# Kernel tuning notes

Hardware: AMD Instinct MI355X
Metric: run time of the kernel (lower is better)

The kernel has to match this reference:

```python
import jax, jax.numpy as jnp
import numpy as np

N_ROWS = 8192
EMBED = 256


def setup_inputs() -> dict:
    key = jax.random.key(0)
    k1, k2, k3, k4, k5 = jax.random.split(key, 5)
    M = jax.random.normal(k1, (N_ROWS, EMBED), dtype=jnp.float32)
    N = jax.random.normal(k2, (N_ROWS, EMBED), dtype=jnp.float32)
    gate_w_weight = jax.random.normal(k3, (1, EMBED), dtype=jnp.float32) * (1.0 / np.sqrt(EMBED))
    gate_w_bias = jax.random.normal(k4, (1,), dtype=jnp.float32)
    gate_b = jax.random.normal(k5, (1,), dtype=jnp.float32)
    return {"M": M, "N": N, "gate_w_weight": gate_w_weight,
            "gate_w_bias": gate_w_bias, "gate_b": gate_b}


def reference(M, N, gate_w_weight, gate_w_bias, gate_b):
    # scores: [n, n] = N @ M^T
    mt = jnp.matmul(N, M.T)
    # zero the diagonal (mt - diag(diag(mt)))
    n = mt.shape[0]
    idx = jnp.arange(n)
    diag_zeroed = mt.at[idx, idx].set(0.0)
    attn = jax.nn.softmax(diag_zeroed, axis=-1)
    out_attn = jnp.matmul(attn, M)  # [n, d]
    # gate: Linear(d -> 1) + extra scalar bias, then sigmoid
    gate_tmp = jnp.matmul(out_attn, gate_w_weight.T) + gate_w_bias + gate_b  # [n, 1]
    gate = jax.nn.sigmoid(gate_tmp)
    boosted = out_attn * gate + N * (1.0 - gate)
    return boosted[:, None, None, :]  # [n, 1, 1, d]
```

## Files before the change

kernel.cpp:

```cpp
#include <hip/hip_runtime.h>
#include <math.h>

#define NR   8192
#define DIM  256
#define QBLK 32

using f32x4  = __attribute__((ext_vector_type(4))) float;
using s4v    = __attribute__((ext_vector_type(4))) short;
using s8v    = __attribute__((ext_vector_type(8))) short;
using bf16x8 = __attribute__((ext_vector_type(8))) short;
typedef _Float16 f16x8 __attribute__((ext_vector_type(8)));
typedef _Float16 f16x4 __attribute__((ext_vector_type(4)));

__device__ __forceinline__ short f2bf(float x){
  union{float f; unsigned u;} v; v.f = x;
  unsigned r = v.u + 0x7fffu + ((v.u >> 16) & 1u);
  return (short)(r >> 16);
}
__device__ __forceinline__ float bf2f(short s){
  union{unsigned u; float f;} v; v.u = ((unsigned)(unsigned short)s) << 16;
  return v.f;
}
__device__ __forceinline__ short f2h(float x){
  union{_Float16 h; short s;} c; c.h = (_Float16)x; return c.s;
}

#define SS_SHORTS 32768
#define WS_BYTES_NEEDED (128u * 32768u * 2u)

#define LDS6_SHORTS 65536

__device__ __forceinline__ void dma16(const short* g, short* l){
  __builtin_amdgcn_global_load_lds(
      (const __attribute__((address_space(1))) unsigned int*)g,
      (__attribute__((address_space(3))) unsigned int*)l, 16, 0, 0);
}

__launch_bounds__(256)
__global__ void precompute_ws(const float* __restrict__ Mp, short* __restrict__ ws)
{
  const int tid = threadIdx.x;
  const int bx  = blockIdx.x;
  const int ss  = bx >> 4;
  const int sub = bx & 15;
  const int fi  = sub*256 + tid;
  const int plane = fi >> 11;
  const int rest  = fi & 2047;
  const int p   = rest >> 10;
  const int cl  = rest & 1023;
  const int ch  = cl >> 6;
  const int l   = cl & 63;
  const int li  = l & 15, g = l >> 4;

  short v[8];
  if (plane == 0){
    const int kk = ch >> 1, n = ch & 1;
    const int row = ss*64 + p*32 + n*16 + li;
    const int d0  = kk*32 + g*8;
    const float* src = Mp + (size_t)row*DIM + d0;
    #pragma unroll
    for (int j = 0; j < 8; ++j) v[j] = f2h(src[j]);
  } else {
    const int u = p*16 + ch;
    #pragma unroll
    for (int j = 0; j < 8; ++j){
      const int fr = u*2 + (l >> 5);
      const int ll = (l & 31)*2 + (j >> 2);
      const int jj = j & 3;
      const int row = ss*64 + (fr >> 4)*16 + (ll >> 4)*4 + jj;
      const int col = (fr & 15)*16 + (ll & 15);
      v[j] = f2h(Mp[(size_t)row*DIM + col]);
    }
  }
  s8v ov = {v[0],v[1],v[2],v[3],v[4],v[5],v[6],v[7]};
  *(s8v*)(ws + (size_t)ss*SS_SHORTS + plane*16384 + p*8192 + ch*512 + l*8) = ov;
}

__launch_bounds__(512, 2)
__global__ void attn_gate_v6(const float* __restrict__ Np,
                             const float* __restrict__ gw, const float* __restrict__ gwb,
                             const float* __restrict__ gb,
                             const short* __restrict__ ws, float* __restrict__ out)
{
  extern __shared__ short S_[];
  const int tid  = threadIdx.x;
  const int w    = tid >> 6;
  const int lane = tid & 63;
  const int g    = lane >> 4;
  const int li   = lane & 15;
  const int qsub = w & 1;
  const int par  = w >> 1;
  const int qb   = blockIdx.x * QBLK;
  const int fbase = w * 8;
  const int fadd  = (w < 4) ? 0 : 16384;

  f16x8 qh[8];
  {
    const float* qrow = Np + (size_t)(qb + qsub*16 + li) * DIM;
    #pragma unroll
    for (int kk = 0; kk < 8; ++kk){
      const int d0 = kk*32 + g*8;
      #pragma unroll
      for (int j = 0; j < 8; ++j)
        qh[kk][j] = (_Float16)qrow[d0 + j];
    }
  }

  f32x4 o[16];
  #pragma unroll
  for (int nf = 0; nf < 16; ++nf){ f32x4 z = {0.f,0.f,0.f,0.f}; o[nf] = z; }
  float m0 = -1e30f, l0 = 0.0f;

  const int p2 = par >> 1, n2 = par & 1;
  const int kfrag_off = p2*8192 + n2*512 + lane*8;

  #pragma unroll
  for (int i = 0; i < 8; ++i){
    const int f = fbase + i;
    dma16(ws + (size_t)f*512 + lane*8, S_ + f*512 + fadd);
  }
  __syncthreads();

  for (int ss = 0; ss < 128; ++ss){
    const size_t ssb = (size_t)ss * SS_SHORTS;
    const int cur = (ss & 1) * 16384;

    if (ss < 127){
      const int nxt = 16384 - cur;
      const size_t nsb = ssb + SS_SHORTS;
      #pragma unroll
      for (int i = 0; i < 8; ++i){
        const int f = fbase + i;
        dma16(ws + nsb + (size_t)f*512 + lane*8, S_ + f*512 + nxt + fadd);
      }
    }

    f32x4 sa0, sa1, sa2, sa3;
    { f32x4 z = {0.f,0.f,0.f,0.f}; sa0 = z; sa1 = z; sa2 = z; sa3 = z; }
    {
      const short* kbase = S_ + cur + kfrag_off;
      __builtin_amdgcn_s_setprio(1);
      #pragma unroll
      for (int kk = 0; kk < 2; ++kk){
        f16x8 bh = *(const f16x8*)(kbase + kk*1024);
        sa0 = __builtin_amdgcn_mfma_f32_16x16x32_f16(bh, qh[kk], sa0, 0, 0, 0);
      }
      #pragma unroll
      for (int kk = 2; kk < 4; ++kk){
        f16x8 bh = *(const f16x8*)(kbase + kk*1024);
        sa1 = __builtin_amdgcn_mfma_f32_16x16x32_f16(bh, qh[kk], sa1, 0, 0, 0);
      }
      #pragma unroll
      for (int kk = 4; kk < 6; ++kk){
        f16x8 bh = *(const f16x8*)(kbase + kk*1024);
        sa2 = __builtin_amdgcn_mfma_f32_16x16x32_f16(bh, qh[kk], sa2, 0, 0, 0);
      }
      #pragma unroll
      for (int kk = 6; kk < 8; ++kk){
        f16x8 bh = *(const f16x8*)(kbase + kk*1024);
        sa3 = __builtin_amdgcn_mfma_f32_16x16x32_f16(bh, qh[kk], sa3, 0, 0, 0);
      }
      __builtin_amdgcn_s_setprio(0);
    }

    const int kvb = ss*64 + par*16 + g*4;
    const int qg  = qb + qsub*16 + li;
    float s_[4];
    #pragma unroll
    for (int i = 0; i < 4; ++i){
      float sv = (sa0[i] + sa1[i]) + (sa2[i] + sa3[i]);
      if (kvb + i == qg) sv = 0.0f;
      s_[i] = sv;
    }
    const float lmax = fmaxf(fmaxf(s_[0], s_[1]), fmaxf(s_[2], s_[3]));
    float sc = 1.0f;
    if (__any((int)(lmax > m0 + 8.0f))){
      float t = lmax;
      t = fmaxf(t, __shfl_xor(t, 16));
      t = fmaxf(t, __shfl_xor(t, 32));
      const float mn = fmaxf(m0, t);
      sc = __expf(m0 - mn);
      m0 = mn;
      float scr[4];
      #pragma unroll
      for (int i = 0; i < 4; ++i) scr[i] = __shfl(sc, g*4 + i);
      #pragma unroll
      for (int nf = 0; nf < 16; ++nf)
        #pragma unroll
        for (int i = 0; i < 4; ++i) o[nf][i] *= scr[i];
    }

    float p_[4];
    #pragma unroll
    for (int i = 0; i < 4; ++i) p_[i] = __expf(s_[i] - m0);

    f16x8 pa;
    pa[0] = (_Float16)p_[0]; pa[1] = (_Float16)p_[1];
    pa[2] = (_Float16)p_[2]; pa[3] = (_Float16)p_[3];
    pa[4] = (_Float16)0.f; pa[5] = (_Float16)0.f;
    pa[6] = (_Float16)0.f; pa[7] = (_Float16)0.f;
    {
      const short* vbase = S_ + 32768 + cur + par*4096 + lane*4;
      __builtin_amdgcn_s_setprio(1);
      #pragma unroll
      for (int nf = 0; nf < 16; ++nf){
        f16x4 b4 = *(const f16x4*)(vbase + nf*256);
        f16x8 bv;
        bv[0] = b4[0]; bv[1] = b4[1]; bv[2] = b4[2]; bv[3] = b4[3];
        bv[4] = (_Float16)0.f; bv[5] = (_Float16)0.f;
        bv[6] = (_Float16)0.f; bv[7] = (_Float16)0.f;
        o[nf] = __builtin_amdgcn_mfma_f32_16x16x32_f16(pa, bv, o[nf], 0, 0, 0);
      }
      __builtin_amdgcn_s_setprio(0);
    }

    float ps = (p_[0] + p_[1]) + (p_[2] + p_[3]);
    ps += __shfl_xor(ps, 16);
    ps += __shfl_xor(ps, 32);
    l0 = l0*sc + ps;

    __syncthreads();
  }

  float mr[4], lr[4];
  #pragma unroll
  for (int i = 0; i < 4; ++i){
    mr[i] = __shfl(m0, g*4 + i);
    lr[i] = __shfl(l0, g*4 + i);
  }

  float* dump = (float*)S_;
  if (par > 0){
    float* dp = dump + (size_t)((par-1)*128 + qsub*64 + lane) * 72;
    #pragma unroll
    for (int i = 0; i < 4; ++i){ dp[i] = mr[i]; dp[4+i] = lr[i]; }
    #pragma unroll
    for (int nf = 0; nf < 16; ++nf)
      #pragma unroll
      for (int i = 0; i < 4; ++i) dp[8 + nf*4 + i] = o[nf][i];
  }
  __syncthreads();
  if (par == 0){
    #pragma unroll
    for (int pp = 0; pp < 3; ++pp){
      const float* dp = dump + (size_t)(pp*128 + qsub*64 + lane) * 72;
      float a[4], b[4];
      #pragma unroll
      for (int i = 0; i < 4; ++i){
        float mb = dp[i], lb = dp[4+i];
        float mm = fmaxf(mr[i], mb);
        a[i] = __expf(mr[i] - mm);
        b[i] = __expf(mb - mm);
        lr[i] = lr[i]*a[i] + lb*b[i];
        mr[i] = mm;
      }
      #pragma unroll
      for (int nf = 0; nf < 16; ++nf)
        #pragma unroll
        for (int i = 0; i < 4; ++i)
          o[nf][i] = o[nf][i]*a[i] + dp[8 + nf*4 + i]*b[i];
    }

    float inv[4];
    #pragma unroll
    for (int i = 0; i < 4; ++i) inv[i] = 1.0f / lr[i];
    #pragma unroll
    for (int nf = 0; nf < 16; ++nf)
      #pragma unroll
      for (int i = 0; i < 4; ++i) o[nf][i] *= inv[i];

    float acc[4] = {0.f, 0.f, 0.f, 0.f};
    #pragma unroll
    for (int nf = 0; nf < 16; ++nf){
      float wv = gw[nf*16 + li];
      #pragma unroll
      for (int i = 0; i < 4; ++i) acc[i] += o[nf][i] * wv;
    }
    const float bias = gwb[0] + gb[0];
    float gt[4];
    #pragma unroll
    for (int i = 0; i < 4; ++i){
      float x = acc[i];
      x += __shfl_xor(x, 1);
      x += __shfl_xor(x, 2);
      x += __shfl_xor(x, 4);
      x += __shfl_xor(x, 8);
      gt[i] = 1.0f / (1.0f + __expf(-(x + bias)));
    }
    #pragma unroll
    for (int i = 0; i < 4; ++i){
      const int grow = qb + qsub*16 + g*4 + i;
      const float* nrow = Np + (size_t)grow * DIM;
      float* orow = out + (size_t)grow * DIM;
      #pragma unroll
      for (int nf = 0; nf < 16; ++nf){
        const int col = nf*16 + li;
        float nv = nrow[col];
        orow[col] = o[nf][i]*gt[i] + nv*(1.0f - gt[i]);
      }
    }
  }
}

#define KH0 0
#define KH1 8448
#define KL0 16896
#define KL1 25344
#define MT0 33792
#define MT1 44032
#define PBO 54272
#define LDS0_SHORTS 56832

__launch_bounds__(256, 1)
__global__ void attn_gate_v0(const float* __restrict__ Mp, const float* __restrict__ Np,
                             const float* __restrict__ gw, const float* __restrict__ gwb,
                             const float* __restrict__ gb, float* __restrict__ out)
{
  extern __shared__ short S_[];
  const int tid  = threadIdx.x;
  const int w    = tid >> 6;
  const int lane = tid & 63;
  const int g    = lane >> 4;
  const int li   = lane & 15;
  const int qsub = w & 1;
  const int par  = w >> 1;
  const int qb   = blockIdx.x * QBLK;

  short* khp = S_ + (par ? KH1 : KH0);
  short* klp = S_ + (par ? KL1 : KL0);
  short* mtp = S_ + (par ? MT1 : MT0);
  short* pb  = S_ + PBO + w * 640;

  bf16x8 qh[8], ql[8];
  {
    const float* qrow = Np + (size_t)(qb + qsub*16 + li) * DIM;
    #pragma unroll
    for (int kk = 0; kk < 8; ++kk){
      const int d0 = kk*32 + g*8;
      #pragma unroll
      for (int j = 0; j < 8; ++j){
        float f = qrow[d0 + j];
        short h = f2bf(f);
        qh[kk][j] = h;
        ql[kk][j] = f2bf(f - bf2f(h));
      }
    }
  }

  f32x4 o[16];
  #pragma unroll
  for (int nf = 0; nf < 16; ++nf){ f32x4 z = {0.f,0.f,0.f,0.f}; o[nf] = z; }
  float m0[4], l0[4];
  #pragma unroll
  for (int i = 0; i < 4; ++i){ m0[i] = -1e30f; l0[i] = 0.0f; }

  const int NSS = NR / 64;
  for (int ss = 0; ss < NSS; ++ss){
    {
      const int r  = tid >> 2;
      const int cb = (tid & 3) << 6;
      const int p  = r >> 5;
      const int rr = r & 31;
      short* kh = S_ + (p ? KH1 : KH0) + rr*264 + cb;
      short* kl = S_ + (p ? KL1 : KL0) + rr*264 + cb;
      short* mt = S_ + (p ? MT1 : MT0) + rr;
      const float* src = Mp + (size_t)(ss*64 + r) * DIM + cb;
      #pragma unroll
      for (int c = 0; c < 64; c += 4){
        const float4 v = *(const float4*)(src + c);
        float fv[4] = {v.x, v.y, v.z, v.w};
        short h[4], lo[4];
        #pragma unroll
        for (int j = 0; j < 4; ++j){
          h[j]  = f2bf(fv[j]);
          lo[j] = f2bf(fv[j] - bf2f(h[j]));
          mt[(cb + c + j) * 40] = h[j];
        }
        s4v hv = {h[0], h[1], h[2], h[3]};
        s4v lv = {lo[0], lo[1], lo[2], lo[3]};
        *(s4v*)(kh + c) = hv;
        *(s4v*)(kl + c) = lv;
      }
    }
    __syncthreads();

    f32x4 sa[2];
    { f32x4 z = {0.f,0.f,0.f,0.f}; sa[0] = z; sa[1] = z; }
    #pragma unroll
    for (int kk = 0; kk < 8; ++kk){
      #pragma unroll
      for (int n = 0; n < 2; ++n){
        const int a = (n*16 + li)*264 + kk*32 + g*8;
        bf16x8 bh = *(const bf16x8*)(khp + a);
        bf16x8 bl = *(const bf16x8*)(klp + a);
        sa[n] = __builtin_amdgcn_mfma_f32_16x16x32_bf16(qh[kk], bh, sa[n], 0, 0, 0);
        sa[n] = __builtin_amdgcn_mfma_f32_16x16x32_bf16(qh[kk], bl, sa[n], 0, 0, 0);
        sa[n] = __builtin_amdgcn_mfma_f32_16x16x32_bf16(ql[kk], bh, sa[n], 0, 0, 0);
      }
    }

    const int kvb   = ss*64 + par*32;
    const int growb = qb + qsub*16 + g*4;
    float s_[2][4];
    #pragma unroll
    for (int n = 0; n < 2; ++n)
      #pragma unroll
      for (int i = 0; i < 4; ++i){
        float sv = sa[n][i];
        if (kvb + n*16 + li == growb + i) sv = 0.0f;
        s_[n][i] = sv;
      }
    float mn[4], sc[4], ps[4];
    bool need = false;
    #pragma unroll
    for (int i = 0; i < 4; ++i){
      float t = fmaxf(s_[0][i], s_[1][i]);
      t = fmaxf(t, __shfl_xor(t, 1));
      t = fmaxf(t, __shfl_xor(t, 2));
      t = fmaxf(t, __shfl_xor(t, 4));
      t = fmaxf(t, __shfl_xor(t, 8));
      mn[i] = fmaxf(m0[i], t);
      sc[i] = __expf(m0[i] - mn[i]);
      need |= (mn[i] != m0[i]);
      m0[i] = mn[i];
    }
    #pragma unroll
    for (int i = 0; i < 4; ++i) ps[i] = 0.0f;
    #pragma unroll
    for (int n = 0; n < 2; ++n)
      #pragma unroll
      for (int i = 0; i < 4; ++i){
        float p = __expf(s_[n][i] - mn[i]);
        ps[i] += p;
        pb[(g*4 + i)*40 + n*16 + li] = f2bf(p);
      }
    #pragma unroll
    for (int i = 0; i < 4; ++i){
      float t = ps[i];
      t += __shfl_xor(t, 1);
      t += __shfl_xor(t, 2);
      t += __shfl_xor(t, 4);
      t += __shfl_xor(t, 8);
      l0[i] = l0[i]*sc[i] + t;
    }
    if (__any((int)need)){
      #pragma unroll
      for (int nf = 0; nf < 16; ++nf)
        #pragma unroll
        for (int i = 0; i < 4; ++i) o[nf][i] *= sc[i];
    }

    bf16x8 pa = *(const bf16x8*)(pb + li*40 + g*8);
    #pragma unroll
    for (int nf = 0; nf < 16; ++nf){
      bf16x8 bv = *(const bf16x8*)(mtp + (nf*16 + li)*40 + g*8);
      o[nf] = __builtin_amdgcn_mfma_f32_16x16x32_bf16(pa, bv, o[nf], 0, 0, 0);
    }
    __syncthreads();
  }

  float* dump = (float*)S_;
  if (par == 1){
    float* dp = dump + (size_t)(qsub*64 + lane) * 72;
    #pragma unroll
    for (int i = 0; i < 4; ++i){ dp[i] = m0[i]; dp[4+i] = l0[i]; }
    #pragma unroll
    for (int nf = 0; nf < 16; ++nf)
      #pragma unroll
      for (int i = 0; i < 4; ++i) dp[8 + nf*4 + i] = o[nf][i];
  }
  __syncthreads();
  if (par == 0){
    const float* dp = dump + (size_t)(qsub*64 + lane) * 72;
    float a[4], b[4];
    #pragma unroll
    for (int i = 0; i < 4; ++i){
      float mb = dp[i], lb = dp[4+i];
      float mm = fmaxf(m0[i], mb);
      a[i] = __expf(m0[i] - mm);
      b[i] = __expf(mb - mm);
      l0[i] = l0[i]*a[i] + lb*b[i];
    }
    #pragma unroll
    for (int nf = 0; nf < 16; ++nf)
      #pragma unroll
      for (int i = 0; i < 4; ++i)
        o[nf][i] = o[nf][i]*a[i] + dp[8 + nf*4 + i]*b[i];

    float inv[4];
    #pragma unroll
    for (int i = 0; i < 4; ++i) inv[i] = 1.0f / l0[i];
    #pragma unroll
    for (int nf = 0; nf < 16; ++nf)
      #pragma unroll
      for (int i = 0; i < 4; ++i) o[nf][i] *= inv[i];

    float t[4] = {0.f, 0.f, 0.f, 0.f};
    #pragma unroll
    for (int nf = 0; nf < 16; ++nf){
      float wv = gw[nf*16 + li];
      #pragma unroll
      for (int i = 0; i < 4; ++i) t[i] += o[nf][i] * wv;
    }
    const float bias = gwb[0] + gb[0];
    float gt[4];
    #pragma unroll
    for (int i = 0; i < 4; ++i){
      float x = t[i];
      x += __shfl_xor(x, 1);
      x += __shfl_xor(x, 2);
      x += __shfl_xor(x, 4);
      x += __shfl_xor(x, 8);
      gt[i] = 1.0f / (1.0f + __expf(-(x + bias)));
    }
    #pragma unroll
    for (int i = 0; i < 4; ++i){
      const int grow = qb + qsub*16 + g*4 + i;
      const float* nrow = Np + (size_t)grow * DIM;
      float* orow = out + (size_t)grow * DIM;
      #pragma unroll
      for (int nf = 0; nf < 16; ++nf){
        const int col = nf*16 + li;
        float nv = nrow[col];
        orow[col] = o[nf][i]*gt[i] + nv*(1.0f - gt[i]);
      }
    }
  }
}

extern "C" void kernel_launch(void* const* d_in, const int* in_sizes, int n_in,
                              void* d_out, int out_size, void* d_ws, size_t ws_size,
                              hipStream_t stream)
{
  const float* Mp  = (const float*)d_in[0];
  const float* Np  = (const float*)d_in[1];
  const float* gw  = (const float*)d_in[2];
  const float* gwb = (const float*)d_in[3];
  const float* gb  = (const float*)d_in[4];
  float* out = (float*)d_out;

  if (ws_size >= (size_t)WS_BYTES_NEEDED){
    short* ws = (short*)d_ws;
    precompute_ws<<<128*16, 256, 0, stream>>>(Mp, ws);
    const size_t shmem = (size_t)LDS6_SHORTS * sizeof(short);
    (void)hipFuncSetAttribute((const void*)attn_gate_v6,
                        hipFuncAttributeMaxDynamicSharedMemorySize, (int)shmem);
    attn_gate_v6<<<NR / QBLK, 512, shmem, stream>>>(Np, gw, gwb, gb, ws, out);
  } else {
    const size_t shmem = (size_t)LDS0_SHORTS * sizeof(short);
    (void)hipFuncSetAttribute((const void*)attn_gate_v0,
                        hipFuncAttributeMaxDynamicSharedMemorySize, (int)shmem);
    attn_gate_v0<<<NR / QBLK, 256, shmem, stream>>>(Mp, Np, gw, gwb, gb, out);
  }
}
```

Measured before the change: 193.7 us.

## Load K fragments straight to registers and use 16x16x16 MFMA for PV

K fragments for the QK^T product are now loaded from global memory directly into double-buffered registers, one chunk ahead, instead of going through LDS. Only the V plane is DMA'd into LDS, which shrinks the LDS footprint. The V layout is reorganised so each lane reads 8 halfs covering two output fragments. PV now uses 16x16x16 MFMAs instead of zero-padded 16x16x32 ones, which halves the wasted MFMA work. In exchange it costs more VGPRs (16 f16x8 registers for K) and adds global-load latency exposure, with redundant K loads across waves sharing the same par.

Measured after the change: 213.3 us. 10.1% more time.

```diff
diff --git a/kernel.cpp b/kernel.cpp
--- a/kernel.cpp
+++ b/kernel.cpp
@@ -28,7 +28,7 @@
 #define SS_SHORTS 32768
 #define WS_BYTES_NEEDED (128u * 32768u * 2u)
 
-#define LDS6_SHORTS 65536
+#define LDS7_SHORTS 55296
 
 __device__ __forceinline__ void dma16(const short* g, short* l){
   __builtin_amdgcn_global_load_lds(
@@ -61,14 +61,15 @@
     #pragma unroll
     for (int j = 0; j < 8; ++j) v[j] = f2h(src[j]);
   } else {
-    const int u = p*16 + ch;
+    const int u   = p*16 + ch;
+    const int par = u >> 3;
+    const int np  = u & 7;
     #pragma unroll
     for (int j = 0; j < 8; ++j){
-      const int fr = u*2 + (l >> 5);
-      const int ll = (l & 31)*2 + (j >> 2);
+      const int nf = 2*np + (j >> 2);
       const int jj = j & 3;
-      const int row = ss*64 + (fr >> 4)*16 + (ll >> 4)*4 + jj;
-      const int col = (fr & 15)*16 + (ll & 15);
+      const int row = ss*64 + par*16 + (l >> 4)*4 + jj;
+      const int col = nf*16 + (l & 15);
       v[j] = f2h(Mp[(size_t)row*DIM + col]);
     }
   }
@@ -77,7 +78,7 @@
 }
 
 __launch_bounds__(512, 2)
-__global__ void attn_gate_v6(const float* __restrict__ Np,
+__global__ void attn_gate_v8(const float* __restrict__ Np,
                              const float* __restrict__ gw, const float* __restrict__ gwb,
                              const float* __restrict__ gb,
                              const short* __restrict__ ws, float* __restrict__ out)
@@ -91,8 +92,6 @@
   const int qsub = w & 1;
   const int par  = w >> 1;
   const int qb   = blockIdx.x * QBLK;
-  const int fbase = w * 8;
-  const int fadd  = (w < 4) ? 0 : 16384;
 
   f16x8 qh[8];
   {
@@ -114,14 +113,21 @@
   const int p2 = par >> 1, n2 = par & 1;
   const int kfrag_off = p2*8192 + n2*512 + lane*8;
 
+  f16x8 khA[8], khB[8];
   #pragma unroll
-  for (int i = 0; i < 8; ++i){
-    const int f = fbase + i;
-    dma16(ws + (size_t)f*512 + lane*8, S_ + f*512 + fadd);
+  for (int i = 0; i < 4; ++i){
+    const int f = w*4 + i;
+    dma16(ws + 16384 + (size_t)f*512 + lane*8, S_ + f*512);
+  }
+  {
+    const short* kb = ws + kfrag_off;
+    #pragma unroll
+    for (int kk = 0; kk < 8; ++kk)
+      khA[kk] = *(const f16x8*)(kb + kk*1024);
   }
   __syncthreads();
 
-  for (int ss = 0; ss < 128; ++ss){
+  auto body = [&](int ss, f16x8 (&khC)[8], f16x8 (&khN)[8]){
     const size_t ssb = (size_t)ss * SS_SHORTS;
     const int cur = (ss & 1) * 16384;
 
@@ -129,39 +135,28 @@
       const int nxt = 16384 - cur;
       const size_t nsb = ssb + SS_SHORTS;
       #pragma unroll
-      for (int i = 0; i < 8; ++i){
-        const int f = fbase + i;
-        dma16(ws + nsb + (size_t)f*512 + lane*8, S_ + f*512 + nxt + fadd);
-      }
+      for (int i = 0; i < 4; ++i){
+        const int f = w*4 + i;
+        dma16(ws + nsb + 16384 + (size_t)f*512 + lane*8, S_ + nxt + f*512);
+      }
+      const short* kb = ws + nsb + kfrag_off;
+      #pragma unroll
+      for (int kk = 0; kk < 8; ++kk)
+        khN[kk] = *(const f16x8*)(kb + kk*1024);
     }
 
     f32x4 sa0, sa1, sa2, sa3;
     { f32x4 z = {0.f,0.f,0.f,0.f}; sa0 = z; sa1 = z; sa2 = z; sa3 = z; }
-    {
-      const short* kbase = S_ + cur + kfrag_off;
-      __builtin_amdgcn_s_setprio(1);
-      #pragma unroll
-      for (int kk = 0; kk < 2; ++kk){
-        f16x8 bh = *(const f16x8*)(kbase + kk*1024);
-        sa0 = __builtin_amdgcn_mfma_f32_16x16x32_f16(bh, qh[kk], sa0, 0, 0, 0);
-      }
-      #pragma unroll
-      for (int kk = 2; kk < 4; ++kk){
-        f16x8 bh = *(const f16x8*)(kbase + kk*1024);
-        sa1 = __builtin_amdgcn_mfma_f32_16x16x32_f16(bh, qh[kk], sa1, 0, 0, 0);
-      }
-      #pragma unroll
-      for (int kk = 4; kk < 6; ++kk){
-        f16x8 bh = *(const f16x8*)(kbase + kk*1024);
-        sa2 = __builtin_amdgcn_mfma_f32_16x16x32_f16(bh, qh[kk], sa2, 0, 0, 0);
-      }
-      #pragma unroll
-      for (int kk = 6; kk < 8; ++kk){
-        f16x8 bh = *(const f16x8*)(kbase + kk*1024);
-        sa3 = __builtin_amdgcn_mfma_f32_16x16x32_f16(bh, qh[kk], sa3, 0, 0, 0);
-      }
-      __builtin_amdgcn_s_setprio(0);
-    }
+    __builtin_amdgcn_s_setprio(1);
+    sa0 = __builtin_amdgcn_mfma_f32_16x16x32_f16(khC[0], qh[0], sa0, 0, 0, 0);
+    sa0 = __builtin_amdgcn_mfma_f32_16x16x32_f16(khC[1], qh[1], sa0, 0, 0, 0);
+    sa1 = __builtin_amdgcn_mfma_f32_16x16x32_f16(khC[2], qh[2], sa1, 0, 0, 0);
+    sa1 = __builtin_amdgcn_mfma_f32_16x16x32_f16(khC[3], qh[3], sa1, 0, 0, 0);
+    sa2 = __builtin_amdgcn_mfma_f32_16x16x32_f16(khC[4], qh[4], sa2, 0, 0, 0);
+    sa2 = __builtin_amdgcn_mfma_f32_16x16x32_f16(khC[5], qh[5], sa2, 0, 0, 0);
+    sa3 = __builtin_amdgcn_mfma_f32_16x16x32_f16(khC[6], qh[6], sa3, 0, 0, 0);
+    sa3 = __builtin_amdgcn_mfma_f32_16x16x32_f16(khC[7], qh[7], sa3, 0, 0, 0);
+    __builtin_amdgcn_s_setprio(0);
 
     const int kvb = ss*64 + par*16 + g*4;
     const int qg  = qb + qsub*16 + li;
@@ -194,22 +189,19 @@
     #pragma unroll
     for (int i = 0; i < 4; ++i) p_[i] = __expf(s_[i] - m0);
 
-    f16x8 pa;
-    pa[0] = (_Float16)p_[0]; pa[1] = (_Float16)p_[1];
-    pa[2] = (_Float16)p_[2]; pa[3] = (_Float16)p_[3];
-    pa[4] = (_Float16)0.f; pa[5] = (_Float16)0.f;
-    pa[6] = (_Float16)0.f; pa[7] = (_Float16)0.f;
+    f16x4 pa4;
+    pa4[0] = (_Float16)p_[0]; pa4[1] = (_Float16)p_[1];
+    pa4[2] = (_Float16)p_[2]; pa4[3] = (_Float16)p_[3];
     {
-      const short* vbase = S_ + 32768 + cur + par*4096 + lane*4;
+      const short* vbase = S_ + cur + par*4096 + lane*8;
       __builtin_amdgcn_s_setprio(1);
       #pragma unroll
-      for (int nf = 0; nf < 16; ++nf){
-        f16x4 b4 = *(const f16x4*)(vbase + nf*256);
-        f16x8 bv;
-        bv[0] = b4[0]; bv[1] = b4[1]; bv[2] = b4[2]; bv[3] = b4[3];
-        bv[4] = (_Float16)0.f; bv[5] = (_Float16)0.f;
-        bv[6] = (_Float16)0.f; bv[7] = (_Float16)0.f;
-        o[nf] = __builtin_amdgcn_mfma_f32_16x16x32_f16(pa, bv, o[nf], 0, 0, 0);
+      for (int np = 0; np < 8; ++np){
+        f16x8 v8 = *(const f16x8*)(vbase + np*512);
+        f16x4 lo; lo[0] = v8[0]; lo[1] = v8[1]; lo[2] = v8[2]; lo[3] = v8[3];
+        f16x4 hi; hi[0] = v8[4]; hi[1] = v8[5]; hi[2] = v8[6]; hi[3] = v8[7];
+        o[2*np]   = __builtin_amdgcn_mfma_f32_16x16x16f16(pa4, lo, o[2*np],   0, 0, 0);
+        o[2*np+1] = __builtin_amdgcn_mfma_f32_16x16x16f16(pa4, hi, o[2*np+1], 0, 0, 0);
       }
       __builtin_amdgcn_s_setprio(0);
     }
@@ -220,6 +212,11 @@
     l0 = l0*sc + ps;
 
     __syncthreads();
+  };
+
+  for (int it = 0; it < 64; ++it){
+    body(2*it,     khA, khB);
+    body(2*it + 1, khB, khA);
   }
 
   float mr[4], lr[4];
@@ -542,10 +539,10 @@
   if (ws_size >= (size_t)WS_BYTES_NEEDED){
     short* ws = (short*)d_ws;
     precompute_ws<<<128*16, 256, 0, stream>>>(Mp, ws);
-    const size_t shmem = (size_t)LDS6_SHORTS * sizeof(short);
-    (void)hipFuncSetAttribute((const void*)attn_gate_v6,
+    const size_t shmem = (size_t)LDS7_SHORTS * sizeof(short);
+    (void)hipFuncSetAttribute((const void*)attn_gate_v8,
                         hipFuncAttributeMaxDynamicSharedMemorySize, (int)shmem);
-    attn_gate_v6<<<NR / QBLK, 512, shmem, stream>>>(Np, gw, gwb, gb, ws, out);
+    attn_gate_v8<<<NR / QBLK, 512, shmem, stream>>>(Np, gw, gwb, gb, ws, out);
   } else {
     const size_t shmem = (size_t)LDS0_SHORTS * sizeof(short);
     (void)hipFuncSetAttribute((const void*)attn_gate_v0,
```
